# Kernel optimization log

Measured on AMD Instinct MI355X. Metric: run time of the kernel, lower is better.

## Reference

```python
import jax, jax.numpy as jnp
import numpy as np

B, N_USERS, N_ITEMS, E, UF, IF = 1024, 1000, 1000, 128, 32, 32
IN_SIZE = E + UF + E + IF  # 320
EPS = 1e-12


def _gru_zero_hidden(x, w_ih, b_ih, b_hh):
    # PyTorch GRUCell with hx=None (zeros): h' = (1-z)*n
    gi = x @ w_ih.T + b_ih                      # (B, 3E)
    i_r, i_z, i_n = jnp.split(gi, 3, axis=1)
    h_r, h_z, h_n = jnp.split(b_hh, 3)
    r = jax.nn.sigmoid(i_r + h_r)
    z = jax.nn.sigmoid(i_z + h_z)
    n = jnp.tanh(i_n + r * h_n)
    return (1.0 - z) * n


def _l2_normalize(x):
    nrm = jnp.sqrt(jnp.sum(x * x, axis=1, keepdims=True))
    return x / jnp.maximum(nrm, EPS)


def setup_inputs() -> dict:
    key = jax.random.key(0)
    ks = jax.random.split(key, 10)
    uid = jax.random.randint(ks[0], (B,), 0, N_USERS)
    iid = jax.random.randint(ks[1], (B,), 0, N_ITEMS)
    feats = jax.random.normal(ks[2], (B, UF + IF), dtype=jnp.float32)
    inputs = jnp.concatenate([uid[:, None].astype(jnp.float32), iid[:, None].astype(jnp.float32), feats], axis=1)
    s = 0.05
    return {
        "inputs": inputs,
        "user_memory": jax.random.normal(ks[3], (B, N_USERS, E), dtype=jnp.float32),
        "item_memory": jax.random.normal(ks[4], (B, N_ITEMS, E), dtype=jnp.float32),
        "w_ih_u": jax.random.normal(ks[5], (3 * E, IN_SIZE), dtype=jnp.float32) * s,
        "b_ih_u": jnp.zeros((3 * E,), dtype=jnp.float32),
        "b_hh_u": jnp.zeros((3 * E,), dtype=jnp.float32),
        "w_ih_i": jax.random.normal(ks[6], (3 * E, IN_SIZE), dtype=jnp.float32) * s,
        "b_ih_i": jnp.zeros((3 * E,), dtype=jnp.float32),
        "b_hh_i": jnp.zeros((3 * E,), dtype=jnp.float32),
    }


def reference(inputs, user_memory, item_memory, w_ih_u, b_ih_u, b_hh_u, w_ih_i, b_ih_i, b_hh_i):
    b = jnp.arange(B)
    user_ids = inputs[:, 0].astype(jnp.int32)
    item_ids = inputs[:, 1].astype(jnp.int32)
    user_features = inputs[:, 2:2 + UF]
    item_features = inputs[:, 2 + UF:]
    # gather per-batch-row memory slots
    um = user_memory[b, user_ids]               # (B, E)
    im = item_memory[b, item_ids]               # (B, E)
    user_inputs = jnp.concatenate([um, user_features, im, item_features], axis=1)
    item_inputs = jnp.concatenate([im, item_features, um, user_features], axis=1)
    new_u = _gru_zero_hidden(user_inputs, w_ih_u, b_ih_u, b_hh_u)
    new_i = _gru_zero_hidden(item_inputs, w_ih_i, b_ih_i, b_hh_i)
    new_u = _l2_normalize(new_u)
    new_i = _l2_normalize(new_i)
    # scatter back into memories
    user_memory = user_memory.at[b, user_ids].set(new_u)
    item_memory = item_memory.at[b, item_ids].set(new_i)
    out = jnp.concatenate([user_ids[:, None].astype(jnp.float32), item_ids[:, None].astype(jnp.float32), new_u, new_i], axis=1)
    return out, user_memory, item_memory
```

## Files before the change

### kernel.cpp

```cpp
#include <hip/hip_runtime.h>
#include <math.h>

#define BATCH 1024
#define NU 1000
#define NI 1000
#define EDIM 128
#define INROW 66
#define IN_SIZE 320
#define OUTROW 258
#define G 4

__global__ __launch_bounds__(256) void limnet_compute(
    const float* __restrict__ inputs,
    const float* __restrict__ umem,
    const float* __restrict__ imem,
    const float* __restrict__ w_u, const float* __restrict__ bih_u, const float* __restrict__ bhh_u,
    const float* __restrict__ w_i, const float* __restrict__ bih_i, const float* __restrict__ bhh_i,
    float* __restrict__ out)
{
    __shared__ float xx[G][640];
    __shared__ float gi[G][768];
    __shared__ float psum[4][G];
    __shared__ int   ids[G][2];

    const int t = threadIdx.x;
    const int wave = t >> 6, lane = t & 63;
    const int b0 = blockIdx.x * G;

    for (int g = 0; g < G; ++g) {
        const int b = b0 + g;
        const float* inrow = inputs + (long)b * INROW;
        const int uid = (int)inrow[0];
        const int iid = (int)inrow[1];
        if (t == 0) { ids[g][0] = uid; ids[g][1] = iid; }
        if (t < 128) {
            float v = umem[((long)b * NU + uid) * EDIM + t];
            xx[g][t]       = v;  xx[g][320 + t] = v;
            float w = imem[((long)b * NI + iid) * EDIM + t];
            xx[g][160 + t] = w;  xx[g][480 + t] = w;
        } else {
            int s = t - 128;
            if (s < 32)      { float v = inrow[2 + s];  xx[g][128 + s] = v; xx[g][448 + s] = v; }
            else if (s < 64) { int s2 = s - 32; float v = inrow[34 + s2]; xx[g][288 + s2] = v; xx[g][608 + s2] = v; }
        }
    }
    __syncthreads();

    const int r0 = wave * 192;
    for (int rr = 0; rr < 192; ++rr) {
        const int row = r0 + rr;
        const float* wrow;
        int xoff;
        if (row < 384) { wrow = w_u + (long)row * IN_SIZE;          xoff = 0;   }
        else           { wrow = w_i + (long)(row - 384) * IN_SIZE;  xoff = 160; }

        float wv[5];
        #pragma unroll
        for (int k5 = 0; k5 < 5; ++k5) wv[k5] = wrow[lane + 64 * k5];

        float p[G];
        #pragma unroll
        for (int g = 0; g < G; ++g) {
            float acc = 0.f;
            #pragma unroll
            for (int k5 = 0; k5 < 5; ++k5)
                acc += wv[k5] * xx[g][xoff + lane + 64 * k5];
            p[g] = acc;
        }
        #pragma unroll
        for (int off = 32; off >= 1; off >>= 1) {
            #pragma unroll
            for (int g = 0; g < G; ++g) p[g] += __shfl_xor(p[g], off);
        }
        if (lane == 0) {
            #pragma unroll
            for (int g = 0; g < G; ++g) gi[g][row] = p[g];
        }
    }
    __syncthreads();

    const int isItem = (t >= 128);
    const int d = isItem ? (t - 128) : t;
    const float* bih = isItem ? bih_i : bih_u;
    const float* bhh = isItem ? bhh_i : bhh_u;
    const float br = bih[d]       + bhh[d];
    const float bz = bih[128 + d] + bhh[128 + d];
    const float bn = bih[256 + d];
    const float hn = bhh[256 + d];
    const int gibase = isItem ? 384 : 0;

    float val[G], ss[G];
    #pragma unroll
    for (int g = 0; g < G; ++g) {
        float ir  = gi[g][gibase + d];
        float iz  = gi[g][gibase + 128 + d];
        float inn = gi[g][gibase + 256 + d];
        float r = 1.f / (1.f + expf(-(ir + br)));
        float z = 1.f / (1.f + expf(-(iz + bz)));
        float n = tanhf(inn + bn + r * hn);
        val[g] = (1.f - z) * n;
        ss[g]  = val[g] * val[g];
    }
    #pragma unroll
    for (int off = 32; off >= 1; off >>= 1) {
        #pragma unroll
        for (int g = 0; g < G; ++g) ss[g] += __shfl_xor(ss[g], off);
    }
    if (lane == 0) {
        #pragma unroll
        for (int g = 0; g < G; ++g) psum[wave][g] = ss[g];
    }
    __syncthreads();

    #pragma unroll
    for (int g = 0; g < G; ++g) {
        float s = isItem ? (psum[2][g] + psum[3][g]) : (psum[0][g] + psum[1][g]);
        float denom = fmaxf(sqrtf(s), 1e-12f);
        float nv = val[g] / denom;
        out[(long)(b0 + g) * OUTROW + 2 + (isItem ? 128 : 0) + d] = nv;
    }
    if (t < 2 * G) {
        int g = t >> 1, col = t & 1;
        out[(long)(b0 + g) * OUTROW + col] = (float)ids[g][col];
    }
}

__global__ __launch_bounds__(256) void limnet_copy(
    const float* __restrict__ mem,
    const float* __restrict__ inputs,
    const float* __restrict__ outbase,
    float* __restrict__ dst,
    int idcol, int newcol)
{
    const int row = blockIdx.x * 8 + (threadIdx.x >> 5);
    const int l   = threadIdx.x & 31;
    const int b   = row / 1000;
    const int n   = row - b * 1000;
    const int id  = (int)inputs[b * INROW + idcol];
    const long off = (long)row * EDIM + l * 4;
    float4 v;
    if (n == id) {
        const float* nr = outbase + (long)b * OUTROW + newcol;
        v = make_float4(nr[l * 4], nr[l * 4 + 1], nr[l * 4 + 2], nr[l * 4 + 3]);
    } else {
        v = *(const float4*)(mem + off);
    }
    *(float4*)(dst + off) = v;
}

extern "C" void kernel_launch(void* const* d_in, const int* in_sizes, int n_in,
                              void* d_out, int out_size, void* d_ws, size_t ws_size,
                              hipStream_t stream) {
    const float* inputs = (const float*)d_in[0];
    const float* umem   = (const float*)d_in[1];
    const float* imem   = (const float*)d_in[2];
    const float* w_u    = (const float*)d_in[3];
    const float* bih_u  = (const float*)d_in[4];
    const float* bhh_u  = (const float*)d_in[5];
    const float* w_i    = (const float*)d_in[6];
    const float* bih_i  = (const float*)d_in[7];
    const float* bhh_i  = (const float*)d_in[8];
    float* out = (float*)d_out;

    limnet_compute<<<BATCH / G, 256, 0, stream>>>(
        inputs, umem, imem, w_u, bih_u, bhh_u, w_i, bih_i, bhh_i, out);

    const long OUTSEC = (long)BATCH * OUTROW;
    const long MEMSZ  = (long)BATCH * NU * EDIM;

    limnet_copy<<<(BATCH * NU) / 8, 256, 0, stream>>>(
        umem, inputs, out, out + OUTSEC, 0, 2);
    limnet_copy<<<(BATCH * NI) / 8, 256, 0, stream>>>(
        imem, inputs, out, out + OUTSEC + MEMSZ, 1, 130);
}
```

Measured before the change: 484.7 us.

## Merge memory copy kernels with nontemporal vector streaming and restructure GRU matvec

The two per-memory copy kernels become one launch over a 2D grid. Each block streams a fifth of a batch row's memory with float4 nontemporal loads and stores, and the per-element id check replaces the per-row divide. The GRU matvec now keeps the inputs in registers as float4 vectors and processes four weight rows per wave in 16-lane groups, which shortens the shuffle reductions. The copy is bandwidth-bound, so the gain depends on cache bypass and fewer launches. The compute change matters little.

Measured after the change: 436.6 us. 9.9% less time.

```diff
diff --git a/kernel.cpp b/kernel.cpp
--- a/kernel.cpp
+++ b/kernel.cpp
@@ -9,6 +9,9 @@
 #define IN_SIZE 320
 #define OUTROW 258
 #define G 4
+#define CHUNKS 5
+
+typedef float f32x4 __attribute__((ext_vector_type(4)));
 
 __global__ __launch_bounds__(256) void limnet_compute(
     const float* __restrict__ inputs,
@@ -25,6 +28,7 @@
 
     const int t = threadIdx.x;
     const int wave = t >> 6, lane = t & 63;
+    const int lane16 = lane & 15, sub = lane >> 4;
     const int b0 = blockIdx.x * G;
 
     for (int g = 0; g < G; ++g) {
@@ -46,35 +50,38 @@
     }
     __syncthreads();
 
-    const int r0 = wave * 192;
-    for (int rr = 0; rr < 192; ++rr) {
-        const int row = r0 + rr;
-        const float* wrow;
-        int xoff;
-        if (row < 384) { wrow = w_u + (long)row * IN_SIZE;          xoff = 0;   }
-        else           { wrow = w_i + (long)(row - 384) * IN_SIZE;  xoff = 160; }
+    const int isItemW = (wave >= 2);
+    const int xoff = isItemW ? 160 : 0;
+    f32x4 xv[G][5];
+    #pragma unroll
+    for (int g = 0; g < G; ++g)
+        #pragma unroll
+        for (int i = 0; i < 5; ++i)
+            xv[g][i] = *(const f32x4*)&xx[g][xoff + lane16 * 4 + i * 64];
 
-        float wv[5];
+    const float* wbase = isItemW ? w_i : w_u;
+    const int rbase = (wave & 1) * 192;
+    const int gibase = isItemW ? 384 : 0;
+    for (int it = 0; it < 48; ++it) {
+        const int row = rbase + it * 4 + sub;
+        const float* wrow = wbase + (long)row * IN_SIZE;
+        float acc[G] = {0.f, 0.f, 0.f, 0.f};
         #pragma unroll
-        for (int k5 = 0; k5 < 5; ++k5) wv[k5] = wrow[lane + 64 * k5];
-
-        float p[G];
-        #pragma unroll
-        for (int g = 0; g < G; ++g) {
-            float acc = 0.f;
+        for (int i = 0; i < 5; ++i) {
+            const f32x4 wv = *(const f32x4*)&wrow[lane16 * 4 + i * 64];
             #pragma unroll
-            for (int k5 = 0; k5 < 5; ++k5)
-                acc += wv[k5] * xx[g][xoff + lane + 64 * k5];
-            p[g] = acc;
+            for (int g = 0; g < G; ++g)
+                acc[g] += wv.x * xv[g][i].x + wv.y * xv[g][i].y
+                        + wv.z * xv[g][i].z + wv.w * xv[g][i].w;
         }
         #pragma unroll
-        for (int off = 32; off >= 1; off >>= 1) {
+        for (int off = 8; off >= 1; off >>= 1) {
             #pragma unroll
-            for (int g = 0; g < G; ++g) p[g] += __shfl_xor(p[g], off);
+            for (int g = 0; g < G; ++g) acc[g] += __shfl_xor(acc[g], off);
         }
-        if (lane == 0) {
+        if (lane16 == 0) {
             #pragma unroll
-            for (int g = 0; g < G; ++g) gi[g][row] = p[g];
+            for (int g = 0; g < G; ++g) gi[g][gibase + row] = acc[g];
         }
     }
     __syncthreads();
@@ -87,14 +94,14 @@
     const float bz = bih[128 + d] + bhh[128 + d];
     const float bn = bih[256 + d];
     const float hn = bhh[256 + d];
-    const int gibase = isItem ? 384 : 0;
+    const int gib = isItem ? 384 : 0;
 
     float val[G], ss[G];
     #pragma unroll
     for (int g = 0; g < G; ++g) {
-        float ir  = gi[g][gibase + d];
-        float iz  = gi[g][gibase + 128 + d];
-        float inn = gi[g][gibase + 256 + d];
+        float ir  = gi[g][gib + d];
+        float iz  = gi[g][gib + 128 + d];
+        float inn = gi[g][gib + 256 + d];
         float r = 1.f / (1.f + expf(-(ir + br)));
         float z = 1.f / (1.f + expf(-(iz + bz)));
         float n = tanhf(inn + bn + r * hn);
@@ -126,26 +133,38 @@
 }
 
 __global__ __launch_bounds__(256) void limnet_copy(
-    const float* __restrict__ mem,
+    const float* __restrict__ umem,
+    const float* __restrict__ imem,
     const float* __restrict__ inputs,
     const float* __restrict__ outbase,
-    float* __restrict__ dst,
-    int idcol, int newcol)
+    float* __restrict__ udst,
+    float* __restrict__ idst)
 {
-    const int row = blockIdx.x * 8 + (threadIdx.x >> 5);
-    const int l   = threadIdx.x & 31;
-    const int b   = row / 1000;
-    const int n   = row - b * 1000;
-    const int id  = (int)inputs[b * INROW + idcol];
-    const long off = (long)row * EDIM + l * 4;
-    float4 v;
-    if (n == id) {
-        const float* nr = outbase + (long)b * OUTROW + newcol;
-        v = make_float4(nr[l * 4], nr[l * 4 + 1], nr[l * 4 + 2], nr[l * 4 + 3]);
-    } else {
-        v = *(const float4*)(mem + off);
+    const int item = blockIdx.y;
+    const int b = blockIdx.x / CHUNKS;
+    const int c = blockIdx.x - b * CHUNKS;
+    const int t = threadIdx.x;
+
+    const f32x4* __restrict__ src4 = (const f32x4*)(item ? imem : umem);
+    f32x4* __restrict__ dst4 = (f32x4*)(item ? idst : udst);
+    const int id = (int)inputs[(long)b * INROW + item];
+    const float* __restrict__ newrow = outbase + (long)b * OUTROW + 2 + item * EDIM;
+
+    const long bbase4 = (long)b * (NU * EDIM / 4);
+    const int  cbase4 = c * 6400;
+
+    #pragma unroll 5
+    for (int i = 0; i < 25; ++i) {
+        const int idx4 = cbase4 + i * 256 + t;
+        const long g4 = bbase4 + idx4;
+        f32x4 v = __builtin_nontemporal_load(&src4[g4]);
+        if ((idx4 >> 5) == id) {
+            const int o = (idx4 & 31) * 4;
+            f32x4 nv = { newrow[o], newrow[o + 1], newrow[o + 2], newrow[o + 3] };
+            v = nv;
+        }
+        __builtin_nontemporal_store(v, &dst4[g4]);
     }
-    *(float4*)(dst + off) = v;
 }
 
 extern "C" void kernel_launch(void* const* d_in, const int* in_sizes, int n_in,
@@ -168,8 +187,7 @@
     const long OUTSEC = (long)BATCH * OUTROW;
     const long MEMSZ  = (long)BATCH * NU * EDIM;
 
-    limnet_copy<<<(BATCH * NU) / 8, 256, 0, stream>>>(
-        umem, inputs, out, out + OUTSEC, 0, 2);
-    limnet_copy<<<(BATCH * NI) / 8, 256, 0, stream>>>(
-        imem, inputs, out, out + OUTSEC + MEMSZ, 1, 130);
+    dim3 cgrid(BATCH * CHUNKS, 2);
+    limnet_copy<<<cgrid, 256, 0, stream>>>(
+        umem, imem, inputs, out, out + OUTSEC, out + OUTSEC + MEMSZ);
 }
```
